# Optimization experiments

Hardware: AMD Instinct MI355X
Metric: run time of the kernel (lower is better)

## Reference

```python
import jax, jax.numpy as jnp
import numpy as np
import math

N_HEADS = 8
EMB = 128
KEY_DIM = EMB // N_HEADS  # 16
B, NQ, T = 32, 1024, 1024


def _uniform(key, shape, stdv):
    return jax.random.uniform(key, shape, jnp.float32, -stdv, stdv)


def setup_inputs() -> dict:
    key = jax.random.key(0)
    ks = jax.random.split(key, 7)
    stdv = 1.0 / math.sqrt(KEY_DIM)      # last dim of w_query/w_key/w_value
    stdv_o = 1.0 / math.sqrt(EMB)        # last dim of w_out
    q = jax.random.normal(ks[0], (B, NQ, EMB), jnp.float32)
    h = jax.random.normal(ks[1], (B, T, EMB), jnp.float32)
    mask = jax.random.randint(ks[2], (B, NQ, T), 0, 2).astype(bool)
    return {
        "q": q,
        "h": h,
        "mask": mask,
        "w_query": _uniform(ks[3], (N_HEADS, EMB, KEY_DIM), stdv),
        "w_key": _uniform(ks[4], (N_HEADS, EMB, KEY_DIM), stdv),
        "w_value": _uniform(ks[5], (N_HEADS, EMB, KEY_DIM), stdv),
        "w_out": _uniform(ks[6], (N_HEADS, KEY_DIM, EMB), stdv_o),
    }


def reference(q, h, mask, w_query, w_key, w_value, w_out):
    # q: [B, NQ, E], h: [B, T, E], mask: [B, NQ, T] (True = blocked)
    scale = 1.0 / math.sqrt(KEY_DIM)
    Q = jnp.einsum('bqi,hik->hbqk', q, w_query)   # [H,B,NQ,dk]
    K = jnp.einsum('bti,hik->hbtk', h, w_key)     # [H,B,T,dk]
    V = jnp.einsum('bti,hiv->hbtv', h, w_value)   # [H,B,T,dv]
    U = scale * jnp.einsum('hbqk,hbtk->hbqt', Q, K)  # [H,B,NQ,T]
    m = mask[None]                                   # broadcast over heads
    U = jnp.where(m, -jnp.inf, U)
    attn = jax.nn.softmax(U, axis=-1)
    attn = jnp.where(m, 0.0, attn)                   # explicit zeroing as in original
    heads = jnp.einsum('hbqt,hbtv->hbqv', attn, V)   # [H,B,NQ,dv]
    out = jnp.einsum('hbqv,hve->bqe', heads, w_out)  # [B,NQ,E]
    return out
```

## Files before the change

### kernel.cpp

```cpp
#include <hip/hip_runtime.h>
#include <hip/hip_bf16.h>
#include <stdint.h>


typedef __attribute__((ext_vector_type(8))) short bf16x8;
typedef __attribute__((ext_vector_type(4))) float f32x4;
typedef __attribute__((ext_vector_type(16))) float f32x16;

#define NEGBIG (-1e30f)
#define QSCALE 0.36067376022224085f
#define EXP2(x) __builtin_amdgcn_exp2f(x)
#define PSTRIDE 68

__device__ __forceinline__ unsigned short f2bf(float x) {
  union { __hip_bfloat16 h; unsigned short u; } cv;
  cv.h = __float2bfloat16(x);
  return cv.u;
}
__device__ __forceinline__ unsigned int pk2bf(float a, float b) {
  unsigned int ua = __float_as_uint(a) + 0x8000u;
  unsigned int ub = __float_as_uint(b) + 0x8000u;
  return __builtin_amdgcn_perm(ub, ua, 0x07060302u);
}
__device__ __forceinline__ unsigned int pk2bf_t(float a, float b) {
  return __builtin_amdgcn_perm(__float_as_uint(b), __float_as_uint(a), 0x07060302u);
}

__global__ __launch_bounds__(256) void projmask_k(const float* __restrict__ qp,
                                                  const float* __restrict__ hp,
                                                  const float* __restrict__ wqp,
                                                  const float* __restrict__ wkp,
                                                  const float* __restrict__ wvp,
                                                  const void* __restrict__ mask,
                                                  unsigned short* __restrict__ Qb,
                                                  unsigned short* __restrict__ Kb,
                                                  unsigned short* __restrict__ Vt,
                                                  unsigned long long* __restrict__ mp64) {
  __shared__ unsigned short WtLds[128 * 136];
  __shared__ __align__(16) unsigned short Cxf[9216];
  const int tid = threadIdx.x;

  if (blockIdx.x >= 1536) {
    const int bx = blockIdx.x - 1536;
    unsigned short* mlds = WtLds;
    const unsigned int* mi = (const unsigned int*)mask;
    unsigned int accv = 0;
    #pragma unroll
    for (int k = 0; k < 16; ++k) accv |= mi[k * 251];
    const bool bytemode = accv > 1u;

    const long long i0 = ((long long)bx * 256 + tid) * 16;
    unsigned int v = 0;
    if (bytemode) {
      int4 w = *(const int4*)((const unsigned char*)mask + i0);
      unsigned int ws[4] = {(unsigned)w.x, (unsigned)w.y, (unsigned)w.z, (unsigned)w.w};
      #pragma unroll
      for (int d = 0; d < 4; ++d) {
        unsigned int t = ws[d] & 0x01010101u;
        v |= ((t * 0x01020408u) >> 24) << (d*4);
      }
    } else {
      const int4* mp4 = (const int4*)((const int*)mask + i0);
      #pragma unroll
      for (int d = 0; d < 4; ++d) {
        int4 w = mp4[d];
        v |= ((unsigned)w.x) << (d*4 + 0);
        v |= ((unsigned)w.y) << (d*4 + 1);
        v |= ((unsigned)w.z) << (d*4 + 2);
        v |= ((unsigned)w.w) << (d*4 + 3);
      }
    }
    mlds[tid] = (unsigned short)v;
    __syncthreads();
    if (tid < 64)
      mp64[(long long)bx * 64 + tid] = ((const unsigned long long*)mlds)[tid];
    return;
  }

  const int wave = tid >> 6, lane = tid & 63;
  const int llo4 = lane & 15, lhi4 = lane >> 4;
  const int xb = blockIdx.x & 511;
  const int sel = blockIdx.x >> 9;
  const int m0 = xb * 64;
  const int b = m0 >> 10, row0 = m0 & 1023;
  const float* A = (sel == 0) ? qp : hp;
  const float* W = (sel == 0) ? wqp : (sel == 1) ? wkp : wvp;
  const float wscale = (sel == 0) ? QSCALE : 1.0f;

  #pragma unroll
  for (int i = 0; i < 8; ++i) {
    int base = (tid + i * 256) * 8;
    float4 w0 = *(const float4*)&W[base];
    float4 w1 = *(const float4*)&W[base + 4];
    float wv8[8] = {w0.x, w0.y, w0.z, w0.w, w1.x, w1.y, w1.z, w1.w};
    #pragma unroll
    for (int j = 0; j < 8; j += 2) {
      unsigned int pk = pk2bf(wv8[j] * wscale, wv8[j+1] * wscale);
      int idx = base + j;
      int h = idx >> 11, e = (idx >> 4) & 127, kk = idx & 15;
      WtLds[(h*16 + kk    ) * 136 + e] = (unsigned short)pk;
      WtLds[(h*16 + kk + 1) * 136 + e] = (unsigned short)(pk >> 16);
    }
  }
  #pragma unroll
  for (int i = 0; i < 4; ++i) {
    int r = (tid >> 4) + i * 16;
    int c = (tid & 15) * 8;
    float4 a0 = *(const float4*)&A[(m0 + r) * 128 + c];
    float4 a1 = *(const float4*)&A[(m0 + r) * 128 + c + 4];
    union { unsigned int u[4]; bf16x8 v; } cvt;
    cvt.u[0] = pk2bf(a0.x, a0.y);
    cvt.u[1] = pk2bf(a0.z, a0.w);
    cvt.u[2] = pk2bf(a1.x, a1.y);
    cvt.u[3] = pk2bf(a1.z, a1.w);
    *(bf16x8*)&Cxf[r * 136 + c] = cvt.v;
  }
  __syncthreads();

  const int n0 = wave * 32;
  f32x4 acc[4][2] = {};
  #pragma unroll
  for (int kk = 0; kk < 128; kk += 32) {
    bf16x8 af[4], bfr[2];
    #pragma unroll
    for (int mi2 = 0; mi2 < 4; ++mi2)
      af[mi2] = *(const bf16x8*)&Cxf[(mi2*16 + llo4)*136 + kk + lhi4*8];
    #pragma unroll
    for (int ni = 0; ni < 2; ++ni)
      bfr[ni] = *(const bf16x8*)&WtLds[(n0 + ni*16 + llo4)*136 + kk + lhi4*8];
    #pragma unroll
    for (int mi2 = 0; mi2 < 4; ++mi2)
      #pragma unroll
      for (int ni = 0; ni < 2; ++ni)
        acc[mi2][ni] = __builtin_amdgcn_mfma_f32_16x16x32_bf16(af[mi2], bfr[ni], acc[mi2][ni], 0, 0, 0);
  }

  __syncthreads();
  if (sel < 2) {
    unsigned short* Cb = sel ? Kb : Qb;
    #pragma unroll
    for (int mi2 = 0; mi2 < 4; ++mi2)
      #pragma unroll
      for (int ni = 0; ni < 2; ++ni) {
        int n = n0 + ni*16 + llo4;
        int rb = (mi2*16 + lhi4*4);
        unsigned int p01 = pk2bf(acc[mi2][ni][0], acc[mi2][ni][1]);
        unsigned int p23 = pk2bf(acc[mi2][ni][2], acc[mi2][ni][3]);
        Cxf[(rb + 0)*136 + n] = (unsigned short)p01;
        Cxf[(rb + 1)*136 + n] = (unsigned short)(p01 >> 16);
        Cxf[(rb + 2)*136 + n] = (unsigned short)p23;
        Cxf[(rb + 3)*136 + n] = (unsigned short)(p23 >> 16);
      }
    __syncthreads();
    #pragma unroll
    for (int it = 0; it < 4; ++it) {
      int u = tid + it*256;
      int h = u >> 7, rk = u & 127, row = rk >> 1, kh = rk & 1;
      bf16x8 vv = *(const bf16x8*)&Cxf[row*136 + h*16 + kh*8];
      *(bf16x8*)&Cb[((b*8 + h)*1024 + row0 + row)*16 + kh*8] = vv;
    }
  } else {
    #pragma unroll
    for (int mi2 = 0; mi2 < 4; ++mi2)
      #pragma unroll
      for (int ni = 0; ni < 2; ++ni) {
        int n = n0 + ni*16 + llo4;
        uint2 pk;
        pk.x = pk2bf(acc[mi2][ni][0], acc[mi2][ni][1]);
        pk.y = pk2bf(acc[mi2][ni][2], acc[mi2][ni][3]);
        *(uint2*)&Cxf[n*72 + mi2*16 + lhi4*4] = pk;
      }
    __syncthreads();
    #pragma unroll
    for (int it = 0; it < 4; ++it) {
      int u = tid + it*256;
      int n = u >> 3, tc = u & 7;
      int h = n >> 4, k = n & 15;
      bf16x8 vv = *(const bf16x8*)&Cxf[n*72 + tc*8];
      *(bf16x8*)&Vt[((b*8 + h)*16 + k)*1024 + row0 + tc*8] = vv;
    }
  }
}

__global__ __launch_bounds__(64) void attn_k(const unsigned short* __restrict__ Qb,
                                             const unsigned short* __restrict__ Kb,
                                             const unsigned short* __restrict__ Vtb,
                                             const unsigned long long* __restrict__ mp64,
                                             unsigned short* __restrict__ heads) {
  __shared__ __align__(16) unsigned short Pw[32 * PSTRIDE];
  __shared__ __align__(8) uint2 mlut[16];
  const int lane = threadIdx.x;
  const int llo4 = lane & 15, lhi4 = lane >> 4;
  const int llo5 = lane & 31, lhi5 = lane >> 5;
  const int bid = blockIdx.x;
  const int nid = (bid & 7) * 512 + (bid >> 3);
  const int q0 = (nid & 15) * 64;
  const int b  = (nid >> 4) & 31;
  const int h  = nid >> 9;
  const int bh = b * 8 + h;
  const unsigned long long* mp_base = &mp64[((b << 10) + q0 + llo5) * 16];
  const unsigned short* Kbase = &Kb[(bh * 1024 + llo5) * 16 + lhi5 * 8];
  const unsigned short* Vbase = &Vtb[(bh * 16 + llo4) * 1024 + lhi4 * 8];

  if (lane < 16) {
    unsigned int n = lane;
    unsigned int h0 = (n & 1u) ? 0u : 0xFFFFu;
    unsigned int h1 = (n & 2u) ? 0u : 0xFFFFu;
    unsigned int h2 = (n & 4u) ? 0u : 0xFFFFu;
    unsigned int h3 = (n & 8u) ? 0u : 0xFFFFu;
    mlut[lane] = make_uint2(h0 | (h1 << 16), h2 | (h3 << 16));
  }

  bf16x8 qf[2];
  #pragma unroll
  for (int qh = 0; qh < 2; ++qh)
    qf[qh] = *(const bf16x8*)&Qb[(bh * 1024 + q0 + qh*32 + llo5) * 16 + lhi5 * 8];

  bf16x8 ones;
  #pragma unroll
  for (int j = 0; j < 8; ++j) ones[j] = (short)0x3F80;
  f32x16 cb16;
  #pragma unroll
  for (int j = 0; j < 16; ++j) cb16[j] = -18.f;

  f32x4 ot[2][2] = {};
  f32x4 lacc[2][2] = {};

  bf16x8 kfb[2][2];
  #pragma unroll
  for (int tt = 0; tt < 2; ++tt)
    kfb[0][tt] = *(const bf16x8*)&Kbase[(tt*32) * 16];

  #pragma unroll 2
  for (int tw = 0; tw < 16; ++tw) {
    const int cur = tw & 1, nxt = cur ^ 1;
    const int twn = (tw < 15) ? tw + 1 : 15;
    const int t0n = twn * 64;
    const int t0  = tw * 64;

    bf16x8 vfb[2];
    #pragma unroll
    for (int kt = 0; kt < 2; ++kt)
      vfb[kt] = *(const bf16x8*)&Vbase[t0 + kt*32];
    unsigned long long mw[2];
    mw[0] = mp_base[tw];
    mw[1] = mp_base[512 + tw];

    #pragma unroll
    for (int tt = 0; tt < 2; ++tt)
      kfb[nxt][tt] = *(const bf16x8*)&Kbase[(t0n + tt*32) * 16];

    #pragma unroll
    for (int qh = 0; qh < 2; ++qh) {
      const unsigned int mwlo = (unsigned int)mw[qh];
      const unsigned int mwhi = (unsigned int)(mw[qh] >> 32);
      #pragma unroll
      for (int tt = 0; tt < 2; ++tt) {
        __builtin_amdgcn_s_setprio(1);
        f32x16 st = __builtin_amdgcn_mfma_f32_32x32x16_bf16(kfb[cur][tt], qf[qh], cb16, 0, 0, 0);
        __builtin_amdgcn_s_setprio(0);
        const unsigned int m32 = (tt ? mwhi : mwlo) >> (lhi5 * 4);
        #pragma unroll
        for (int g = 0; g < 4; ++g) {
          unsigned int nib = (m32 >> (g*8)) & 0xFu;
          uint2 am = mlut[nib];
          uint2 d;
          d.x = pk2bf_t(EXP2(st[g*4 + 0]), EXP2(st[g*4 + 1])) & am.x;
          d.y = pk2bf_t(EXP2(st[g*4 + 2]), EXP2(st[g*4 + 3])) & am.y;
          *(uint2*)&Pw[llo5 * PSTRIDE + tt*32 + lhi5*4 + g*8] = d;
        }
      }

      __builtin_amdgcn_s_setprio(1);
      #pragma unroll
      for (int kt = 0; kt < 2; ++kt) {
        #pragma unroll
        for (int qn = 0; qn < 2; ++qn) {
          const unsigned short* pp = &Pw[(qn*16 + llo4) * PSTRIDE + kt*32 + lhi4*8];
          uint2 p0 = *(const uint2*)pp;
          uint2 p1 = *(const uint2*)(pp + 4);
          union { uint2 u[2]; bf16x8 v; } pf;
          pf.u[0] = p0; pf.u[1] = p1;
          ot[qh][qn]   = __builtin_amdgcn_mfma_f32_16x16x32_bf16(vfb[kt], pf.v, ot[qh][qn], 0, 0, 0);
          lacc[qh][qn] = __builtin_amdgcn_mfma_f32_16x16x32_bf16(ones,    pf.v, lacc[qh][qn], 0, 0, 0);
        }
      }
      __builtin_amdgcn_s_setprio(0);
    }
  }

  #pragma unroll
  for (int qh = 0; qh < 2; ++qh)
    #pragma unroll
    for (int qn = 0; qn < 2; ++qn) {
      float l = lacc[qh][qn][0];
      float inv = l > 0.f ? 1.f / l : 0.f;
      f32x4 o = ot[qh][qn] * inv;
      uint2 d;
      d.x = pk2bf(o[0], o[1]);
      d.y = pk2bf(o[2], o[3]);
      *(uint2*)&heads[((b << 10) + q0 + qh*32 + qn*16 + llo4) * 128 + h*16 + lhi4*4] = d;
    }
}

__global__ __launch_bounds__(256) void outproj_k(const unsigned short* __restrict__ Av,
                                                 const float* __restrict__ W,
                                                 float* __restrict__ Co) {
  __shared__ unsigned short WtLds[128 * 136];
  __shared__ __align__(16) unsigned short Cxf[9216];
  const int tid = threadIdx.x;
  const int wave = tid >> 6, lane = tid & 63;
  const int llo4 = lane & 15, lhi4 = lane >> 4;
  const int m0 = blockIdx.x * 64;

  #pragma unroll
  for (int i = 0; i < 8; ++i) {
    int base = (tid + i * 256) * 8;
    float4 w0 = *(const float4*)&W[base];
    float4 w1 = *(const float4*)&W[base + 4];
    float wv8[8] = {w0.x, w0.y, w0.z, w0.w, w1.x, w1.y, w1.z, w1.w};
    #pragma unroll
    for (int j = 0; j < 8; j += 2) {
      unsigned int pk = pk2bf(wv8[j], wv8[j+1]);
      int idx = base + j;
      WtLds[((idx & 127)    ) * 136 + (idx >> 7)] = (unsigned short)pk;
      WtLds[((idx & 127) + 1) * 136 + (idx >> 7)] = (unsigned short)(pk >> 16);
    }
  }
  #pragma unroll
  for (int i = 0; i < 4; ++i) {
    int r = (tid >> 4) + i * 16;
    int c = (tid & 15) * 8;
    *(bf16x8*)&Cxf[r * 136 + c] = *(const bf16x8*)&Av[(m0 + r) * 128 + c];
  }
  __syncthreads();

  const int n0 = wave * 32;
  f32x4 acc[4][2] = {};
  #pragma unroll
  for (int kk = 0; kk < 128; kk += 32) {
    bf16x8 af[4], bfr[2];
    #pragma unroll
    for (int mi2 = 0; mi2 < 4; ++mi2)
      af[mi2] = *(const bf16x8*)&Cxf[(mi2*16 + llo4)*136 + kk + lhi4*8];
    #pragma unroll
    for (int ni = 0; ni < 2; ++ni)
      bfr[ni] = *(const bf16x8*)&WtLds[(n0 + ni*16 + llo4)*136 + kk + lhi4*8];
    #pragma unroll
    for (int mi2 = 0; mi2 < 4; ++mi2)
      #pragma unroll
      for (int ni = 0; ni < 2; ++ni)
        acc[mi2][ni] = __builtin_amdgcn_mfma_f32_16x16x32_bf16(af[mi2], bfr[ni], acc[mi2][ni], 0, 0, 0);
  }
  #pragma unroll
  for (int mi2 = 0; mi2 < 4; ++mi2)
    #pragma unroll
    for (int ni = 0; ni < 2; ++ni) {
      int n = n0 + ni*16 + llo4;
      int mbase = m0 + mi2*16 + lhi4*4;
      #pragma unroll
      for (int r = 0; r < 4; ++r)
        Co[(mbase + r) * 128 + n] = acc[mi2][ni][r];
    }
}

extern "C" void kernel_launch(void* const* d_in, const int* in_sizes, int n_in,
                              void* d_out, int out_size, void* d_ws, size_t ws_size,
                              hipStream_t stream) {
  const float* q  = (const float*)d_in[0];
  const float* hh = (const float*)d_in[1];
  const void*  mk = d_in[2];
  const float* wq = (const float*)d_in[3];
  const float* wk = (const float*)d_in[4];
  const float* wv = (const float*)d_in[5];
  const float* wo = (const float*)d_in[6];
  float* out = (float*)d_out;

  unsigned short* Qb = (unsigned short*)d_ws;
  unsigned short* Kb = Qb + 32*8*1024*16;
  unsigned short* Vt = Kb + 32*8*1024*16;
  unsigned short* hd = Vt + 32*8*1024*16;
  unsigned long long* mp64 = (unsigned long long*)(hd + 32768*128);

  projmask_k<<<9728, 256, 0, stream>>>(q, hh, wq, wk, wv, mk, Qb, Kb, Vt, mp64);
  attn_k<<<4096, 64, 0, stream>>>(Qb, Kb, Vt, mp64, hd);
  outproj_k<<<512, 256, 0, stream>>>(hd, wo, out);
}
```

Baseline: 296.1 us.

## Share K/V tiles across four waves via double-buffered LDS in attention

The attention kernel now runs 256-thread blocks, with four waves each handling 64 queries of the same (batch, head). K and V tiles are loaded cooperatively into double-buffered LDS and shared by all waves, instead of every wave reading them from global memory itself. This cuts redundant global/L2 traffic for K and V by about 4x. In exchange it adds a block-wide barrier every tile, fewer and larger blocks (1024 instead of 4096), and extra LDS reads per iteration.

```diff
diff --git a/kernel.cpp b/kernel.cpp
--- a/kernel.cpp
+++ b/kernel.cpp
@@ -11,6 +11,8 @@
 #define QSCALE 0.36067376022224085f
 #define EXP2(x) __builtin_amdgcn_exp2f(x)
 #define PSTRIDE 68
+#define KST 20
+#define VST 68
 
 __device__ __forceinline__ unsigned short f2bf(float x) {
   union { __hip_bfloat16 h; unsigned short u; } cv;
@@ -182,39 +184,53 @@
   }
 }
 
-__global__ __launch_bounds__(64) void attn_k(const unsigned short* __restrict__ Qb,
-                                             const unsigned short* __restrict__ Kb,
-                                             const unsigned short* __restrict__ Vtb,
-                                             const unsigned long long* __restrict__ mp64,
-                                             unsigned short* __restrict__ heads) {
-  __shared__ __align__(16) unsigned short Pw[32 * PSTRIDE];
+__global__ __launch_bounds__(256) void attn_k(const unsigned short* __restrict__ Qb,
+                                              const unsigned short* __restrict__ Kb,
+                                              const unsigned short* __restrict__ Vtb,
+                                              const unsigned long long* __restrict__ mp64,
+                                              unsigned short* __restrict__ heads) {
+  __shared__ __align__(16) unsigned short Klds[2][64 * KST];
+  __shared__ __align__(16) unsigned short Vlds[2][16 * VST];
+  __shared__ __align__(16) unsigned short Pw[4][32 * PSTRIDE];
   __shared__ __align__(8) uint2 mlut[16];
-  const int lane = threadIdx.x;
+  const int tid  = threadIdx.x;
+  const int wave = tid >> 6, lane = tid & 63;
   const int llo4 = lane & 15, lhi4 = lane >> 4;
   const int llo5 = lane & 31, lhi5 = lane >> 5;
   const int bid = blockIdx.x;
-  const int nid = (bid & 7) * 512 + (bid >> 3);
-  const int q0 = (nid & 15) * 64;
-  const int b  = (nid >> 4) & 31;
-  const int h  = nid >> 9;
+  const int nid = (bid & 7) * 128 + (bid >> 3);
+  const int qblk = nid & 3;
+  const int bhid = nid >> 2;
+  const int b = bhid & 31, h = bhid >> 5;
   const int bh = b * 8 + h;
-  const unsigned long long* mp_base = &mp64[((b << 10) + q0 + llo5) * 16];
-  const unsigned short* Kbase = &Kb[(bh * 1024 + llo5) * 16 + lhi5 * 8];
-  const unsigned short* Vbase = &Vtb[(bh * 16 + llo4) * 1024 + lhi4 * 8];
-
-  if (lane < 16) {
-    unsigned int n = lane;
+  const int q0w = qblk * 256 + wave * 64;
+
+  if (tid < 16) {
+    unsigned int n = tid;
     unsigned int h0 = (n & 1u) ? 0u : 0xFFFFu;
     unsigned int h1 = (n & 2u) ? 0u : 0xFFFFu;
     unsigned int h2 = (n & 4u) ? 0u : 0xFFFFu;
     unsigned int h3 = (n & 8u) ? 0u : 0xFFFFu;
-    mlut[lane] = make_uint2(h0 | (h1 << 16), h2 | (h3 << 16));
-  }
-
+    mlut[tid] = make_uint2(h0 | (h1 << 16), h2 | (h3 << 16));
+  }
+
+  const bool isK = (wave < 2);
+  const int krow = (wave & 1) * 32 + (lane >> 1);
+  const int kkh  = (lane & 1) * 8;
+  const int vk   = (wave & 1) * 8 + (lane >> 3);
+  const int vc   = (lane & 7) * 8;
+  const unsigned short* sg = isK ? (Kb + bh * 16384 + krow * 16 + kkh)
+                                 : (Vtb + (bh * 16 + vk) * 1024 + vc);
+  const int sg_step = isK ? 1024 : 64;
+  unsigned short* sd = isK ? &Klds[0][krow * KST + kkh]
+                           : &Vlds[0][vk * VST + vc];
+  const int sd_step = isK ? (64 * KST) : (16 * VST);
+
+  const unsigned long long* mp_base = &mp64[((b << 10) + q0w + llo5) * 16];
   bf16x8 qf[2];
   #pragma unroll
   for (int qh = 0; qh < 2; ++qh)
-    qf[qh] = *(const bf16x8*)&Qb[(bh * 1024 + q0 + qh*32 + llo5) * 16 + lhi5 * 8];
+    qf[qh] = *(const bf16x8*)&Qb[(bh * 1024 + q0w + qh*32 + llo5) * 16 + lhi5 * 8];
 
   bf16x8 ones;
   #pragma unroll
@@ -226,38 +242,56 @@
   f32x4 ot[2][2] = {};
   f32x4 lacc[2][2] = {};
 
-  bf16x8 kfb[2][2];
-  #pragma unroll
-  for (int tt = 0; tt < 2; ++tt)
-    kfb[0][tt] = *(const bf16x8*)&Kbase[(tt*32) * 16];
+  unsigned short* PwW = &Pw[wave][0];
+
+  {
+    union { bf16x8 v; uint2 u[2]; } sp;
+    sp.v = *(const bf16x8*)sg;
+    *(uint2*)sd = sp.u[0];
+    *(uint2*)(sd + 4) = sp.u[1];
+  }
+  unsigned long long mreg0 = mp_base[0];
+  unsigned long long mreg1 = mp_base[512];
+  __syncthreads();
 
   #pragma unroll 2
   for (int tw = 0; tw < 16; ++tw) {
     const int cur = tw & 1, nxt = cur ^ 1;
-    const int twn = (tw < 15) ? tw + 1 : 15;
-    const int t0n = twn * 64;
-    const int t0  = tw * 64;
-
-    bf16x8 vfb[2];
-    #pragma unroll
-    for (int kt = 0; kt < 2; ++kt)
-      vfb[kt] = *(const bf16x8*)&Vbase[t0 + kt*32];
-    unsigned long long mw[2];
-    mw[0] = mp_base[tw];
-    mw[1] = mp_base[512 + tw];
-
-    #pragma unroll
-    for (int tt = 0; tt < 2; ++tt)
-      kfb[nxt][tt] = *(const bf16x8*)&Kbase[(t0n + tt*32) * 16];
+    bf16x8 sregn;
+    unsigned long long mregn0 = 0, mregn1 = 0;
+    if (tw < 15) {
+      sregn = *(const bf16x8*)(sg + (tw + 1) * sg_step);
+      mregn0 = mp_base[tw + 1];
+      mregn1 = mp_base[512 + tw + 1];
+      __builtin_amdgcn_sched_barrier(0);
+    }
+
+    bf16x8 kf[2], vf[2];
+    {
+      const unsigned short* kb0 = &Klds[cur][llo5 * KST + lhi5 * 8];
+      union { uint2 u[2]; bf16x8 v; } k0u, k1u, v0u, v1u;
+      k0u.u[0] = *(const uint2*)(kb0);
+      k0u.u[1] = *(const uint2*)(kb0 + 4);
+      k1u.u[0] = *(const uint2*)(kb0 + 32 * KST);
+      k1u.u[1] = *(const uint2*)(kb0 + 32 * KST + 4);
+      kf[0] = k0u.v; kf[1] = k1u.v;
+      const unsigned short* vb0 = &Vlds[cur][llo4 * VST + lhi4 * 8];
+      v0u.u[0] = *(const uint2*)(vb0);
+      v0u.u[1] = *(const uint2*)(vb0 + 4);
+      v1u.u[0] = *(const uint2*)(vb0 + 32);
+      v1u.u[1] = *(const uint2*)(vb0 + 32 + 4);
+      vf[0] = v0u.v; vf[1] = v1u.v;
+    }
 
     #pragma unroll
     for (int qh = 0; qh < 2; ++qh) {
-      const unsigned int mwlo = (unsigned int)mw[qh];
-      const unsigned int mwhi = (unsigned int)(mw[qh] >> 32);
+      const unsigned long long mw = qh ? mreg1 : mreg0;
+      const unsigned int mwlo = (unsigned int)mw;
+      const unsigned int mwhi = (unsigned int)(mw >> 32);
       #pragma unroll
       for (int tt = 0; tt < 2; ++tt) {
         __builtin_amdgcn_s_setprio(1);
-        f32x16 st = __builtin_amdgcn_mfma_f32_32x32x16_bf16(kfb[cur][tt], qf[qh], cb16, 0, 0, 0);
+        f32x16 st = __builtin_amdgcn_mfma_f32_32x32x16_bf16(kf[tt], qf[qh], cb16, 0, 0, 0);
         __builtin_amdgcn_s_setprio(0);
         const unsigned int m32 = (tt ? mwhi : mwlo) >> (lhi5 * 4);
         #pragma unroll
@@ -267,7 +301,7 @@
           uint2 d;
           d.x = pk2bf_t(EXP2(st[g*4 + 0]), EXP2(st[g*4 + 1])) & am.x;
           d.y = pk2bf_t(EXP2(st[g*4 + 2]), EXP2(st[g*4 + 3])) & am.y;
-          *(uint2*)&Pw[llo5 * PSTRIDE + tt*32 + lhi5*4 + g*8] = d;
+          *(uint2*)&PwW[llo5 * PSTRIDE + tt*32 + lhi5*4 + g*8] = d;
         }
       }
 
@@ -276,16 +310,25 @@
       for (int kt = 0; kt < 2; ++kt) {
         #pragma unroll
         for (int qn = 0; qn < 2; ++qn) {
-          const unsigned short* pp = &Pw[(qn*16 + llo4) * PSTRIDE + kt*32 + lhi4*8];
+          const unsigned short* pp = &PwW[(qn*16 + llo4) * PSTRIDE + kt*32 + lhi4*8];
           uint2 p0 = *(const uint2*)pp;
           uint2 p1 = *(const uint2*)(pp + 4);
           union { uint2 u[2]; bf16x8 v; } pf;
           pf.u[0] = p0; pf.u[1] = p1;
-          ot[qh][qn]   = __builtin_amdgcn_mfma_f32_16x16x32_bf16(vfb[kt], pf.v, ot[qh][qn], 0, 0, 0);
-          lacc[qh][qn] = __builtin_amdgcn_mfma_f32_16x16x32_bf16(ones,    pf.v, lacc[qh][qn], 0, 0, 0);
+          ot[qh][qn]   = __builtin_amdgcn_mfma_f32_16x16x32_bf16(vf[kt], pf.v, ot[qh][qn], 0, 0, 0);
+          lacc[qh][qn] = __builtin_amdgcn_mfma_f32_16x16x32_bf16(ones,   pf.v, lacc[qh][qn], 0, 0, 0);
         }
       }
       __builtin_amdgcn_s_setprio(0);
+    }
+
+    if (tw < 15) {
+      union { bf16x8 v; uint2 u[2]; } sp;
+      sp.v = sregn;
+      *(uint2*)(sd + nxt * sd_step) = sp.u[0];
+      *(uint2*)(sd + nxt * sd_step + 4) = sp.u[1];
+      mreg0 = mregn0; mreg1 = mregn1;
+      __syncthreads();
     }
   }
 
@@ -299,7 +342,7 @@
       uint2 d;
       d.x = pk2bf(o[0], o[1]);
       d.y = pk2bf(o[2], o[3]);
-      *(uint2*)&heads[((b << 10) + q0 + qh*32 + qn*16 + llo4) * 128 + h*16 + lhi4*4] = d;
+      *(uint2*)&heads[((b << 10) + q0w + qh*32 + qn*16 + llo4) * 128 + h*16 + lhi4*4] = d;
     }
 }
 
@@ -383,6 +426,6 @@
   unsigned long long* mp64 = (unsigned long long*)(hd + 32768*128);
 
   projmask_k<<<9728, 256, 0, stream>>>(q, hh, wq, wk, wv, mk, Qb, Kb, Vt, mp64);
-  attn_k<<<4096, 64, 0, stream>>>(Qb, Kb, Vt, mp64, hd);
+  attn_k<<<1024, 256, 0, stream>>>(Qb, Kb, Vt, mp64, hd);
   outproj_k<<<512, 256, 0, stream>>>(hd, wo, out);
 }
```

Result: no change. 301.4 us (+1.8%).

## Pack mask with 64 elements per thread and double-buffer attention P tile

Applied to the files above, without the earlier changes.

The mask-packing blocks now have each thread process 64 mask elements and write a full 64-bit word directly to global memory. This removes the LDS staging and block barrier and cuts the mask block count from 8192 to 2048. Separately, the attention kernel gets two P buffers, one per query half, so writes for the second half need not wait on reads of the first. This relieves LDS write-after-read hazards at the cost of doubling the P tile's shared memory.

```diff
diff --git a/kernel.cpp b/kernel.cpp
--- a/kernel.cpp
+++ b/kernel.cpp
@@ -42,38 +42,45 @@
 
   if (blockIdx.x >= 1536) {
     const int bx = blockIdx.x - 1536;
-    unsigned short* mlds = WtLds;
     const unsigned int* mi = (const unsigned int*)mask;
     unsigned int accv = 0;
     #pragma unroll
     for (int k = 0; k < 16; ++k) accv |= mi[k * 251];
     const bool bytemode = accv > 1u;
 
-    const long long i0 = ((long long)bx * 256 + tid) * 16;
-    unsigned int v = 0;
+    const long long i0 = ((long long)bx * 256 + tid) * 64;
+    unsigned long long out = 0;
     if (bytemode) {
-      int4 w = *(const int4*)((const unsigned char*)mask + i0);
-      unsigned int ws[4] = {(unsigned)w.x, (unsigned)w.y, (unsigned)w.z, (unsigned)w.w};
-      #pragma unroll
-      for (int d = 0; d < 4; ++d) {
-        unsigned int t = ws[d] & 0x01010101u;
-        v |= ((t * 0x01020408u) >> 24) << (d*4);
+      const int4* mp4 = (const int4*)((const unsigned char*)mask + i0);
+      #pragma unroll
+      for (int j = 0; j < 4; ++j) {
+        int4 w = mp4[j];
+        unsigned int ws[4] = {(unsigned)w.x, (unsigned)w.y, (unsigned)w.z, (unsigned)w.w};
+        unsigned long long v = 0;
+        #pragma unroll
+        for (int d = 0; d < 4; ++d) {
+          unsigned int t = ws[d] & 0x01010101u;
+          v |= (unsigned long long)((t * 0x01020408u) >> 24) << (d*4);
+        }
+        out |= v << (j*16);
       }
     } else {
       const int4* mp4 = (const int4*)((const int*)mask + i0);
       #pragma unroll
-      for (int d = 0; d < 4; ++d) {
-        int4 w = mp4[d];
-        v |= ((unsigned)w.x) << (d*4 + 0);
-        v |= ((unsigned)w.y) << (d*4 + 1);
-        v |= ((unsigned)w.z) << (d*4 + 2);
-        v |= ((unsigned)w.w) << (d*4 + 3);
-      }
-    }
-    mlds[tid] = (unsigned short)v;
-    __syncthreads();
-    if (tid < 64)
-      mp64[(long long)bx * 64 + tid] = ((const unsigned long long*)mlds)[tid];
+      for (int j = 0; j < 4; ++j) {
+        unsigned long long v = 0;
+        #pragma unroll
+        for (int d = 0; d < 4; ++d) {
+          int4 w = mp4[j*4 + d];
+          v |= ((unsigned long long)(unsigned)w.x) << (d*4 + 0);
+          v |= ((unsigned long long)(unsigned)w.y) << (d*4 + 1);
+          v |= ((unsigned long long)(unsigned)w.z) << (d*4 + 2);
+          v |= ((unsigned long long)(unsigned)w.w) << (d*4 + 3);
+        }
+        out |= v << (j*16);
+      }
+    }
+    mp64[(long long)bx * 256 + tid] = out;
     return;
   }
 
@@ -187,7 +194,7 @@
                                              const unsigned short* __restrict__ Vtb,
                                              const unsigned long long* __restrict__ mp64,
                                              unsigned short* __restrict__ heads) {
-  __shared__ __align__(16) unsigned short Pw[32 * PSTRIDE];
+  __shared__ __align__(16) unsigned short Pw[2][32 * PSTRIDE];
   __shared__ __align__(8) uint2 mlut[16];
   const int lane = threadIdx.x;
   const int llo4 = lane & 15, lhi4 = lane >> 4;
@@ -252,6 +259,7 @@
 
     #pragma unroll
     for (int qh = 0; qh < 2; ++qh) {
+      unsigned short* PwW = &Pw[qh][0];
       const unsigned int mwlo = (unsigned int)mw[qh];
       const unsigned int mwhi = (unsigned int)(mw[qh] >> 32);
       #pragma unroll
@@ -267,7 +275,7 @@
           uint2 d;
           d.x = pk2bf_t(EXP2(st[g*4 + 0]), EXP2(st[g*4 + 1])) & am.x;
           d.y = pk2bf_t(EXP2(st[g*4 + 2]), EXP2(st[g*4 + 3])) & am.y;
-          *(uint2*)&Pw[llo5 * PSTRIDE + tt*32 + lhi5*4 + g*8] = d;
+          *(uint2*)&PwW[llo5 * PSTRIDE + tt*32 + lhi5*4 + g*8] = d;
         }
       }
 
@@ -276,7 +284,7 @@
       for (int kt = 0; kt < 2; ++kt) {
         #pragma unroll
         for (int qn = 0; qn < 2; ++qn) {
-          const unsigned short* pp = &Pw[(qn*16 + llo4) * PSTRIDE + kt*32 + lhi4*8];
+          const unsigned short* pp = &PwW[(qn*16 + llo4) * PSTRIDE + kt*32 + lhi4*8];
           uint2 p0 = *(const uint2*)pp;
           uint2 p1 = *(const uint2*)(pp + 4);
           union { uint2 u[2]; bf16x8 v; } pf;
@@ -382,7 +390,7 @@
   unsigned short* hd = Vt + 32*8*1024*16;
   unsigned long long* mp64 = (unsigned long long*)(hd + 32768*128);
 
-  projmask_k<<<9728, 256, 0, stream>>>(q, hh, wq, wk, wv, mk, Qb, Kb, Vt, mp64);
+  projmask_k<<<3584, 256, 0, stream>>>(q, hh, wq, wk, wv, mk, Qb, Kb, Vt, mp64);
   attn_k<<<4096, 64, 0, stream>>>(Qb, Kb, Vt, mp64, hd);
   outproj_k<<<512, 256, 0, stream>>>(hd, wo, out);
 }
```

Result: no change. 299.7 us (+1.2%).
